# Kernel optimization log

Hardware: AMD Instinct MI355X
Metric: run time of the kernel (lower is better)

## Reference

```python
import jax, jax.numpy as jnp
import numpy as np


def setup_inputs() -> dict:
    key = jax.random.key(0)
    N, E, H, V, C, D, L = 10000, 50000, 128, 8, 5, 59, 2
    keys = iter(jax.random.split(key, 64))

    def p(*shape):
        return jax.random.normal(next(keys), shape, jnp.float32) * 0.05

    inp = dict(
        edge_index=jax.random.randint(next(keys), (2, E), 0, N),
        edge_attr=jax.random.normal(next(keys), (E, D), jnp.float32),
        delta_t=jnp.array([60.0], jnp.float32),
        memory=jnp.ones((N, H), jnp.float32),
        # edge_embed
        W_ee=p(H, D), b_ee=p(H),
        # edge_weight_gen
        W_ewg=p(V, 2 * H), b_ewg=p(V),
        # multi-view GIN convs (L layers, shared MLP across views)
        gin_W1=p(L, H, H), gin_b1=p(L, H), gin_W2=p(L, H, H), gin_b2=p(L, H),
        # Bochner time encoder
        W_t=p(H, 1), b_t=p(H),
        # GRUCell (torch gate order r,z,n)
        W_ih=p(3 * H, H), b_ih=p(3 * H), W_hh=p(3 * H, H), b_hh=p(3 * H),
        # update_nn (feeds detached memory only; not in returned outputs)
        W_up=p(H, V * H), b_up=p(H),
        # local attention (kdim=vdim=2H, 1 head)
        Wq_l=p(H, H), bq_l=p(H), Wk_l=p(H, 2 * H), bk_l=p(H),
        Wv_l=p(H, 2 * H), bv_l=p(H), Wo_l=p(H, H), bo_l=p(H),
        # global attention (1 head)
        Wq_g=p(H, H), bq_g=p(H), Wk_g=p(H, H), bk_g=p(H),
        Wv_g=p(H, H), bv_g=p(H), Wo_g=p(H, H), bo_g=p(H),
        # classifier MLP
        Wc1=p(H, 3 * H), bc1=p(H), Wc2=p(C, H), bc2=p(C),
    )
    return inp


def reference(edge_index, edge_attr, delta_t, memory,
              W_ee, b_ee, W_ewg, b_ewg,
              gin_W1, gin_b1, gin_W2, gin_b2,
              W_t, b_t, W_ih, b_ih, W_hh, b_hh, W_up, b_up,
              Wq_l, bq_l, Wk_l, bk_l, Wv_l, bv_l, Wo_l, bo_l,
              Wq_g, bq_g, Wk_g, bk_g, Wv_g, bv_g, Wo_g, bo_g,
              Wc1, bc1, Wc2, bc2):
    relu = jax.nn.relu
    N, H = memory.shape
    V = W_ewg.shape[0]
    L = gin_W1.shape[0]

    # ---- snapshot encoder (MultiGraphLayer) ----
    ea = relu(edge_attr @ W_ee.T + b_ee)                               # [E,H]
    src0, dst0 = edge_index[0], edge_index[1]
    ew = jax.nn.sigmoid(
        jnp.concatenate([ea, memory[src0]], -1) @ W_ewg.T + b_ewg)     # [E,V]
    h = jnp.broadcast_to(memory[:, None, :], (N, V, H))                # [N,V,H]
    cs, cd = dst0, src0  # edge_index flipped before convs (edge_index[[1,0]])
    for l in range(L):
        # multi-view GIN: view-weighted message + residual MLP update
        msg = relu(h[cs] + ea[:, None, :]) * ew[:, :, None]            # [E,V,H]
        agg = jax.ops.segment_sum(msg, cd, num_segments=N)             # [N,V,H]
        upd = relu((h + agg) @ gin_W1[l].T + gin_b1[l]) @ gin_W2[l].T + gin_b2[l]
        h = h + upd
    h_before = h

    # ---- GRU memory update (vectorized over the V 'class' slots) ----
    te = jnp.sin(delta_t[:, None] * W_t[:, 0] + b_t)                   # [1,H]
    x_in = h + te                                                      # [N,V,H]
    gi = x_in @ W_ih.T + b_ih                                          # [N,V,3H]
    gh = (memory @ W_hh.T + b_hh)[:, None, :]                          # [N,1,3H]
    r = jax.nn.sigmoid(gi[..., :H] + gh[..., :H])
    z = jax.nn.sigmoid(gi[..., H:2 * H] + gh[..., H:2 * H])
    n = jnp.tanh(gi[..., 2 * H:] + r * gh[..., 2 * H:])
    h_new = (1.0 - z) * n + z * memory[:, None, :]                     # [N,V,H]

    # ---- global/local attention fusion ----
    scale = 1.0 / jnp.sqrt(jnp.asarray(H, jnp.float32))
    sf, df = h_new[src0], h_new[dst0]                                  # [E,V,H]
    Wk1, Wk2 = Wk_l[:, :H], Wk_l[:, H:]  # split cat([src,dst]) projection
    Wv1, Wv2 = Wv_l[:, :H], Wv_l[:, H:]
    q_l = ea @ Wq_l.T + bq_l                                           # [E,H]
    K_l = sf @ Wk1.T + df @ Wk2.T + bk_l                               # [E,V,H]
    V_l = sf @ Wv1.T + df @ Wv2.T + bv_l
    a_l = jax.nn.softmax(jnp.einsum('eh,evh->ev', q_l, K_l) * scale, -1)
    local_out = jnp.einsum('ev,evh->eh', a_l, V_l) @ Wo_l.T + bo_l     # [E,H]

    pooled = h_new.mean(axis=0)                                        # [V,H]
    q_g = ea @ Wq_g.T + bq_g
    K_g = pooled @ Wk_g.T + bk_g
    V_g = pooled @ Wv_g.T + bv_g
    a_g = jax.nn.softmax((q_g @ K_g.T) * scale, axis=-1)               # [E,V]
    global_out = (a_g @ V_g) @ Wo_g.T + bo_g                           # [E,H]

    combined = jnp.concatenate([ea, local_out, global_out], axis=-1)   # [E,3H]
    logits = relu(combined @ Wc1.T + bc1) @ Wc2.T + bc2                # [E,C]
    return (logits, ew, h_before, a_g[:, None, :])
```

## Files before the change

kernel.cpp:

```cpp
#include <hip/hip_runtime.h>
#include <cstddef>


#define HSZ 128
typedef unsigned short ushortT;
typedef unsigned int uintT;
typedef short short8 __attribute__((ext_vector_type(8)));
typedef float f32x4 __attribute__((ext_vector_type(4)));

__device__ __forceinline__ float sigm(float x) { return 1.f / (1.f + __expf(-x)); }

__device__ __forceinline__ ushortT f2bf(float f) {
  unsigned int u = __float_as_uint(f);
  u += 0x7fffu + ((u >> 16) & 1u);
  return (ushortT)(u >> 16);
}
__device__ __forceinline__ float bf2f(ushortT u) {
  return __uint_as_float(((unsigned int)u) << 16);
}
__device__ __forceinline__ float bflo(uintT u) { return __uint_as_float(u << 16); }
__device__ __forceinline__ float bfhi(uintT u) { return __uint_as_float(u & 0xffff0000u); }
__device__ __forceinline__ uintT pk2bf(float a, float b) {
  return ((uintT)f2bf(b) << 16) | (uintT)f2bf(a);
}

__device__ __forceinline__ int swzA(int row, int chunk) {
  return row * 64 + (((chunk ^ row) & 7) << 3);
}
__device__ __forceinline__ int swzT(int row, int chunk) {
  return row * 128 + (((chunk & 8) | ((chunk ^ row) & 7)) << 3);
}

template<int ASRC, int ACT, bool OUTBF, bool ABF, bool WBF>
__global__ __launch_bounds__(256) void gemm_bf(
    const void* __restrict__ A1, const void* __restrict__ A2, const void* __restrict__ A3,
    const void* __restrict__ W, const float* __restrict__ bias,
    void* __restrict__ out_, int M, int K, int Nout)
{
  __shared__ short Ash[128 * 64];
  __shared__ short Bsh[128 * 64];
  float* out = (float*)out_;
  ushortT* outh = (ushortT*)out_;
  const int tid = threadIdx.x;
  const int m0 = blockIdx.x * 128;
  const int n0 = blockIdx.y * 128;
  const int l = tid & 63, w = tid >> 6;
  const int wr = w >> 1, wc = w & 1;
  const int lr = l & 15, lq = l >> 4;
  f32x4 acc[4][4] = {};

  for (int k0 = 0; k0 < K; k0 += 64) {
    __syncthreads();
    const bool fast = (k0 + 64 <= K);
    #pragma unroll
    for (int i = 0; i < 4; ++i) {
      int c = i * 256 + tid;
      int row = c >> 3, seg = c & 7;
      int kb = k0 + seg * 8;
      {
        int m = m0 + row;
        short8 pk;
        if (ABF) {
          if (m < M) {
            if (ASRC == 4) {
              if (kb < 128)
                pk = *reinterpret_cast<const short8*>((const ushortT*)A1 + (size_t)m * 128 + kb);
              else if (kb < 384)
                pk = *reinterpret_cast<const short8*>((const ushortT*)A2 + (size_t)m * 256 + (kb - 128));
              else
                pk = *reinterpret_cast<const short8*>((const ushortT*)A3 + (size_t)m * 128 + (kb - 384));
            } else {
              pk = *reinterpret_cast<const short8*>((const ushortT*)A1 + (size_t)m * K + kb);
            }
          } else {
            #pragma unroll
            for (int j = 0; j < 8; ++j) pk[j] = 0;
          }
        } else {
          const float* A1f = (const float*)A1;
          float v[8];
          if (fast && m < M) {
            const float4* p = reinterpret_cast<const float4*>(A1f + (size_t)m * K + kb);
            float4 x0 = p[0], x1 = p[1];
            v[0]=x0.x; v[1]=x0.y; v[2]=x0.z; v[3]=x0.w;
            v[4]=x1.x; v[5]=x1.y; v[6]=x1.z; v[7]=x1.w;
          } else {
            #pragma unroll
            for (int j = 0; j < 8; ++j) {
              int k = kb + j;
              v[j] = (m < M && k < K) ? A1f[(size_t)m * K + k] : 0.f;
            }
          }
          #pragma unroll
          for (int j = 0; j < 8; ++j) pk[j] = (short)f2bf(v[j]);
        }
        *reinterpret_cast<short8*>(&Ash[swzA(row, seg)]) = pk;
      }
      {
        int nn = n0 + row;
        short8 pk;
        if (WBF) {
          if (nn < Nout)
            pk = *reinterpret_cast<const short8*>((const ushortT*)W + (size_t)nn * K + kb);
          else {
            #pragma unroll
            for (int j = 0; j < 8; ++j) pk[j] = 0;
          }
        } else {
          const float* Wf = (const float*)W;
          float v[8];
          if (fast && nn < Nout) {
            const float4* p = reinterpret_cast<const float4*>(Wf + (size_t)nn * K + kb);
            float4 x0 = p[0], x1 = p[1];
            v[0]=x0.x; v[1]=x0.y; v[2]=x0.z; v[3]=x0.w;
            v[4]=x1.x; v[5]=x1.y; v[6]=x1.z; v[7]=x1.w;
          } else {
            #pragma unroll
            for (int j = 0; j < 8; ++j) {
              int k = kb + j;
              v[j] = (nn < Nout && k < K) ? Wf[(size_t)nn * K + k] : 0.f;
            }
          }
          #pragma unroll
          for (int j = 0; j < 8; ++j) pk[j] = (short)f2bf(v[j]);
        }
        *reinterpret_cast<short8*>(&Bsh[swzA(row, seg)]) = pk;
      }
    }
    __syncthreads();
    #pragma unroll
    for (int ks = 0; ks < 2; ++ks) {
      short8 a[4], b[4];
      #pragma unroll
      for (int mi = 0; mi < 4; ++mi)
        a[mi] = *reinterpret_cast<const short8*>(&Ash[swzA(wr*64 + mi*16 + lr, ks*4 + lq)]);
      #pragma unroll
      for (int ni = 0; ni < 4; ++ni)
        b[ni] = *reinterpret_cast<const short8*>(&Bsh[swzA(wc*64 + ni*16 + lr, ks*4 + lq)]);
      #pragma unroll
      for (int mi = 0; mi < 4; ++mi)
        #pragma unroll
        for (int ni = 0; ni < 4; ++ni)
          acc[mi][ni] = __builtin_amdgcn_mfma_f32_16x16x32_bf16(a[mi], b[ni], acc[mi][ni], 0, 0, 0);
    }
  }
  #pragma unroll
  for (int ni = 0; ni < 4; ++ni) {
    int col = n0 + wc*64 + ni*16 + lr;
    if (col >= Nout) continue;
    float bz = bias ? bias[col] : 0.f;
    #pragma unroll
    for (int mi = 0; mi < 4; ++mi) {
      int mb = m0 + wr*64 + mi*16 + lq*4;
      #pragma unroll
      for (int r = 0; r < 4; ++r) {
        int m = mb + r;
        if (m >= M) continue;
        float vv = acc[mi][ni][r] + bz;
        if (ACT == 1) vv = fmaxf(vv, 0.f);
        size_t o = (size_t)m * Nout + col;
        if (OUTBF) outh[o] = f2bf(vv); else out[o] = vv;
      }
    }
  }
}

template<int LMODE>
__global__ __launch_bounds__(256) void k_gin(
    const ushortT* __restrict__ hb, const ushortT* __restrict__ aggb,
    float* __restrict__ houtf, ushortT* __restrict__ houtb,
    const ushortT* __restrict__ W1b, const float* __restrict__ b1,
    const ushortT* __restrict__ W2b, const float* __restrict__ b2, int M)
{
  __shared__ short Tsh[16384];
  const int tid = threadIdx.x;
  const int m0 = blockIdx.x * 128;
  const int l = tid & 63, w = tid >> 6;
  const int wr = w >> 1, wc = w & 1;
  const int lr = l & 15, lq = l >> 4;
  f32x4 acc[4][4] = {};

  #pragma unroll
  for (int kk = 0; kk < 4; ++kk) {
    const int kof = kk * 32 + lq * 8;
    short8 a[4], b[4];
    #pragma unroll
    for (int mi = 0; mi < 4; ++mi) {
      int m = m0 + wr*64 + mi*16 + lr;
      if (m < M) {
        short8 hv;
        if (LMODE == 1) hv = *reinterpret_cast<const short8*>(hb + ((size_t)(m >> 3)) * 128 + kof);
        else            hv = *reinterpret_cast<const short8*>(hb + (size_t)m * 128 + kof);
        short8 av = *reinterpret_cast<const short8*>(aggb + (size_t)m * 128 + kof);
        #pragma unroll
        for (int j = 0; j < 8; ++j)
          a[mi][j] = (short)f2bf(bf2f((ushortT)hv[j]) + bf2f((ushortT)av[j]));
      } else {
        #pragma unroll
        for (int j = 0; j < 8; ++j) a[mi][j] = 0;
      }
    }
    #pragma unroll
    for (int ni = 0; ni < 4; ++ni)
      b[ni] = *reinterpret_cast<const short8*>(W1b + (size_t)(wc*64 + ni*16 + lr) * 128 + kof);
    #pragma unroll
    for (int mi = 0; mi < 4; ++mi)
      #pragma unroll
      for (int ni = 0; ni < 4; ++ni)
        acc[mi][ni] = __builtin_amdgcn_mfma_f32_16x16x32_bf16(a[mi], b[ni], acc[mi][ni], 0, 0, 0);
  }
  {
    float b1v[4];
    #pragma unroll
    for (int ni = 0; ni < 4; ++ni) b1v[ni] = b1[wc*64 + ni*16 + lr];
    #pragma unroll
    for (int mi = 0; mi < 4; ++mi)
      #pragma unroll
      for (int ni = 0; ni < 4; ++ni) {
        int col = wc*64 + ni*16 + lr;
        #pragma unroll
        for (int r = 0; r < 4; ++r) {
          int row = wr*64 + mi*16 + lq*4 + r;
          float v = fmaxf(acc[mi][ni][r] + b1v[ni], 0.f);
          Tsh[swzT(row, col >> 3) + (col & 7)] = (short)f2bf(v);
        }
      }
  }
  __syncthreads();
  f32x4 acc2[4][4] = {};
  #pragma unroll
  for (int kk = 0; kk < 4; ++kk) {
    const int kof = kk * 32 + lq * 8;
    short8 a[4], b[4];
    #pragma unroll
    for (int mi = 0; mi < 4; ++mi)
      a[mi] = *reinterpret_cast<const short8*>(&Tsh[swzT(wr*64 + mi*16 + lr, kk*4 + lq)]);
    #pragma unroll
    for (int ni = 0; ni < 4; ++ni)
      b[ni] = *reinterpret_cast<const short8*>(W2b + (size_t)(wc*64 + ni*16 + lr) * 128 + kof);
    #pragma unroll
    for (int mi = 0; mi < 4; ++mi)
      #pragma unroll
      for (int ni = 0; ni < 4; ++ni)
        acc2[mi][ni] = __builtin_amdgcn_mfma_f32_16x16x32_bf16(a[mi], b[ni], acc2[mi][ni], 0, 0, 0);
  }
  {
    float b2v[4];
    #pragma unroll
    for (int ni = 0; ni < 4; ++ni) b2v[ni] = b2[wc*64 + ni*16 + lr];
    #pragma unroll
    for (int ni = 0; ni < 4; ++ni) {
      int col = wc*64 + ni*16 + lr;
      #pragma unroll
      for (int mi = 0; mi < 4; ++mi) {
        int mb = m0 + wr*64 + mi*16 + lq*4;
        #pragma unroll
        for (int r = 0; r < 4; ++r) {
          int m = mb + r;
          if (m >= M) continue;
          float base = (LMODE == 1) ? bf2f(hb[((size_t)(m >> 3)) * 128 + col])
                                    : bf2f(hb[(size_t)m * 128 + col]);
          float ho = base + acc2[mi][ni][r] + b2v[ni];
          if (LMODE == 1) houtb[(size_t)m * 128 + col] = f2bf(ho);
          else            houtf[(size_t)m * 128 + col] = ho;
        }
      }
    }
  }
}

__global__ __launch_bounds__(512) void k_giru(
    const float* __restrict__ hf, const float* __restrict__ te,
    const ushortT* __restrict__ Wihb, const float* __restrict__ b_ih,
    const ushortT* __restrict__ ghb, const ushortT* __restrict__ memb,
    ushortT* __restrict__ hnb, float* __restrict__ prw, int M)
{
  __shared__ short Ash[8192];
  __shared__ float poolsh[1024];
  const int tid = threadIdx.x;
  const int m0 = blockIdx.x * 64;
  const int l = tid & 63, w = tid >> 6;
  const int lr = l & 15, lq = l >> 4;
  const int r0 = (w >> 1) * 16, c0 = (w & 1) * 64;
  f32x4 acc[3][4] = {};

  #pragma unroll
  for (int i = 0; i < 2; ++i) {
    int c = i * 512 + tid;
    int row = c >> 4, seg = c & 15;
    int m = m0 + row;
    short8 pk;
    if (m < M) {
      const float4* p = reinterpret_cast<const float4*>(hf + (size_t)m * 128 + seg * 8);
      const float4* t = reinterpret_cast<const float4*>(te + seg * 8);
      float4 x0 = p[0], x1 = p[1], t0 = t[0], t1 = t[1];
      pk[0]=(short)f2bf(x0.x+t0.x); pk[1]=(short)f2bf(x0.y+t0.y);
      pk[2]=(short)f2bf(x0.z+t0.z); pk[3]=(short)f2bf(x0.w+t0.w);
      pk[4]=(short)f2bf(x1.x+t1.x); pk[5]=(short)f2bf(x1.y+t1.y);
      pk[6]=(short)f2bf(x1.z+t1.z); pk[7]=(short)f2bf(x1.w+t1.w);
    } else {
      #pragma unroll
      for (int j = 0; j < 8; ++j) pk[j] = 0;
    }
    *reinterpret_cast<short8*>(&Ash[swzT(row, seg)]) = pk;
  }
  for (int i = tid; i < 1024; i += 512) poolsh[i] = 0.f;
  __syncthreads();
  #pragma unroll
  for (int kk = 0; kk < 4; ++kk) {
    short8 a = *reinterpret_cast<const short8*>(&Ash[swzT(r0 + lr, kk*4 + lq)]);
    #pragma unroll
    for (int s = 0; s < 3; ++s)
      #pragma unroll
      for (int xi = 0; xi < 4; ++xi) {
        short8 b = *reinterpret_cast<const short8*>(
            Wihb + (size_t)(s*128 + c0 + xi*16 + lr) * 128 + kk*32 + lq*8);
        acc[s][xi] = __builtin_amdgcn_mfma_f32_16x16x32_bf16(a, b, acc[s][xi], 0, 0, 0);
      }
  }
  #pragma unroll
  for (int xi = 0; xi < 4; ++xi) {
    int x = c0 + xi * 16 + lr;
    float br = b_ih[x], bz = b_ih[128 + x], bn = b_ih[256 + x];
    #pragma unroll
    for (int rr = 0; rr < 4; ++rr) {
      int m = m0 + r0 + lq * 4 + rr;
      if (m >= M) continue;
      int node = m >> 3;
      float ghr = bf2f(ghb[(size_t)node * 384 + x]);
      float ghz = bf2f(ghb[(size_t)node * 384 + 128 + x]);
      float ghn = bf2f(ghb[(size_t)node * 384 + 256 + x]);
      float mem = bf2f(memb[(size_t)node * 128 + x]);
      float rv = sigm(acc[0][xi][rr] + br + ghr);
      float zv = sigm(acc[1][xi][rr] + bz + ghz);
      float nv = tanhf(acc[2][xi][rr] + bn + rv * ghn);
      float hn = (1.f - zv) * nv + zv * mem;
      hnb[(size_t)m * 128 + x] = f2bf(hn);
      atomicAdd(&poolsh[(m & 7) * 128 + x], hn);
    }
  }
  __syncthreads();
  for (int i = tid; i < 1024; i += 512) atomicAdd(&prw[i], poolsh[i]);
}

__global__ void k_hist(const int* __restrict__ srcI, int* __restrict__ cnt, int E)
{
  int e = blockIdx.x * 256 + threadIdx.x;
  if (e < E) atomicAdd(&cnt[srcI[e]], 1);
}

__global__ __launch_bounds__(1024) void k_scan(const int* __restrict__ cnt,
    int* __restrict__ ofs, int* __restrict__ cur, int N)
{
  __shared__ int buf[1024];
  __shared__ int carry;
  int tid = threadIdx.x;
  if (tid == 0) carry = 0;
  __syncthreads();
  for (int base = 0; base < N; base += 1024) {
    int i = base + tid;
    int v = (i < N) ? cnt[i] : 0;
    buf[tid] = v;
    __syncthreads();
    for (int off = 1; off < 1024; off <<= 1) {
      int t = (tid >= off) ? buf[tid - off] : 0;
      __syncthreads();
      buf[tid] += t;
      __syncthreads();
    }
    int excl = carry + buf[tid] - v;
    if (i < N) { ofs[i] = excl; cur[i] = excl; }
    __syncthreads();
    if (tid == 0) carry += buf[1023];
    __syncthreads();
  }
  if (tid == 0) ofs[N] = carry;
}

__global__ void k_fill(const int* __restrict__ srcI, int* __restrict__ cur,
                       int* __restrict__ eid, int E)
{
  int e = blockIdx.x * 256 + threadIdx.x;
  if (e >= E) return;
  int p = atomicAdd(&cur[srcI[e]], 1);
  eid[p] = e;
}

template<int LMODE>
__global__ __launch_bounds__(256) void k_agg(const ushortT* __restrict__ hb,
    const ushortT* __restrict__ eab, const float* __restrict__ ew,
    const int* __restrict__ dstI, const int* __restrict__ ofs,
    const int* __restrict__ eid, ushortT* __restrict__ aggb, int N)
{
  int half = threadIdx.x >> 7;
  int x = threadIdx.x & 127;
  int n = blockIdx.x * 2 + half;
  if (n >= N) return;
  float acc[8] = {};
  int beg = ofs[n], end = ofs[n + 1];
  for (int i = beg; i < end; ++i) {
    int e = eid[i];
    int d = dstI[e];
    float eav = bf2f(eab[(size_t)e * 128 + x]);
    const float* ewp = ew + (size_t)e * 8;
    if (LMODE == 1) {
      float m = fmaxf(bf2f(hb[(size_t)d * 128 + x]) + eav, 0.f);
      #pragma unroll
      for (int v = 0; v < 8; ++v) acc[v] += m * ewp[v];
    } else {
      const ushortT* hd = hb + (size_t)d * 1024;
      #pragma unroll
      for (int v = 0; v < 8; ++v)
        acc[v] += fmaxf(bf2f(hd[v * 128 + x]) + eav, 0.f) * ewp[v];
    }
  }
  ushortT* ag = aggb + (size_t)n * 1024;
  #pragma unroll
  for (int v = 0; v < 8; ++v) ag[v * 128 + x] = f2bf(acc[v]);
}

__global__ __launch_bounds__(256) void k_ew(const ushortT* __restrict__ eab,
    const ushortT* __restrict__ memb, const int* __restrict__ srcI,
    const float* __restrict__ W_ewg, const float* __restrict__ b_ewg,
    float* __restrict__ ew, int E)
{
  __shared__ float Wsh[2048];
  __shared__ float bsh[8];
  int tid = threadIdx.x;
  for (int i = tid; i < 2048; i += 256) Wsh[i] = W_ewg[i];
  if (tid < 8) bsh[tid] = b_ewg[tid];
  __syncthreads();
  int wv = tid >> 6, lane = tid & 63;
  int e = blockIdx.x * 4 + wv;
  if (e >= E) return;
  int s = srcI[e];
  float c0 = bf2f(eab[(size_t)e * 128 + lane]);
  float c1 = bf2f(eab[(size_t)e * 128 + 64 + lane]);
  float c2 = bf2f(memb[(size_t)s * 128 + lane]);
  float c3 = bf2f(memb[(size_t)s * 128 + 64 + lane]);
  #pragma unroll
  for (int v = 0; v < 8; ++v) {
    float p = c0 * Wsh[v * 256 + lane] + c1 * Wsh[v * 256 + 64 + lane]
            + c2 * Wsh[v * 256 + 128 + lane] + c3 * Wsh[v * 256 + 192 + lane];
    #pragma unroll
    for (int o = 32; o; o >>= 1) p += __shfl_down(p, o);
    if (lane == 0) ew[(size_t)e * 8 + v] = sigm(p + bsh[v]);
  }
}

__global__ void k_cvtall(const float* __restrict__ s0, ushortT* __restrict__ d0, int n0,
                         const float* __restrict__ s1, ushortT* __restrict__ d1, int n1,
                         const float* __restrict__ s2, ushortT* __restrict__ d2, int n2,
                         const float* __restrict__ s3, ushortT* __restrict__ d3, int n3)
{
  int i = blockIdx.x * 256 + threadIdx.x;
  if (i < n0) { d0[i] = f2bf(s0[i]); return; }
  i -= n0;
  if (i < n1) { d1[i] = f2bf(s1[i]); return; }
  i -= n1;
  if (i < n2) { d2[i] = f2bf(s2[i]); return; }
  i -= n2;
  if (i < n3) d3[i] = f2bf(s3[i]);
}

__global__ __launch_bounds__(256) void k_prep(
    const float* __restrict__ Wo_l, const float* __restrict__ Wv_l,
    const float* __restrict__ bv_l, const float* __restrict__ bo_l,
    const float* __restrict__ Wq_l, const float* __restrict__ bq_l,
    const float* __restrict__ Wk_l,
    const float* __restrict__ delta_t, const float* __restrict__ W_t,
    const float* __restrict__ b_t,
    float* __restrict__ Wl2f, float* __restrict__ blv,
    ushortT* __restrict__ Wqkgb, float* __restrict__ bqkg, float* __restrict__ te)
{
  int idx = blockIdx.x * 256 + threadIdx.x;
  if (idx < 32768) {
    int n = idx >> 8, k = idx & 255;
    float a = 0.f;
    for (int j = 0; j < 128; ++j) a += Wo_l[n * 128 + j] * Wv_l[j * 256 + k];
    Wl2f[idx] = a;
  } else {
    int rem = idx - 32768;
    int n = rem >> 7, j = rem & 127;
    float a = 0.f;
    for (int k = 0; k < 128; ++k) a += Wq_l[k * 128 + j] * Wk_l[k * 256 + n];
    Wqkgb[rem] = f2bf(a);
  }
  if (blockIdx.x == 0 && threadIdx.x < 128) {
    int n = threadIdx.x;
    float a = bo_l[n];
    for (int j = 0; j < 128; ++j) a += Wo_l[n * 128 + j] * bv_l[j];
    blv[n] = a;
  }
  if (blockIdx.x == 1) {
    int n = threadIdx.x;
    float a = 0.f;
    for (int k = 0; k < 128; ++k) a += bq_l[k] * Wk_l[k * 256 + n];
    bqkg[n] = a;
  }
  if (blockIdx.x == 2 && threadIdx.x < 128) {
    int t = threadIdx.x;
    te[t] = sinf(delta_t[0] * W_t[t] + b_t[t]);
  }
}

__global__ __launch_bounds__(256) void k_prep2(
    const float* __restrict__ Wc1, const float* __restrict__ bc1,
    const float* __restrict__ Wl2f, const float* __restrict__ blv,
    ushortT* __restrict__ Wc1p, float* __restrict__ bc1p)
{
  int idx = blockIdx.x * 256 + threadIdx.x;
  int n = idx >> 9, k = idx & 511;
  float a;
  if (k < 128) a = Wc1[(size_t)n * 384 + k];
  else if (k < 384) {
    int kk = k - 128;
    a = 0.f;
    for (int j = 0; j < 128; ++j) a += Wc1[(size_t)n * 384 + 128 + j] * Wl2f[j * 256 + kk];
  } else a = Wc1[(size_t)n * 384 + 256 + (k - 384)];
  Wc1p[idx] = f2bf(a);
  if (blockIdx.x == 0 && threadIdx.x < 128) {
    int nn = threadIdx.x;
    float b = bc1[nn];
    for (int j = 0; j < 128; ++j) b += Wc1[(size_t)nn * 384 + 128 + j] * blv[j];
    bc1p[nn] = b;
  }
}

__global__ __launch_bounds__(256) void k_kgg(const float* __restrict__ prw,
    const float* __restrict__ Wk_g, const float* __restrict__ Wv_g, const float* __restrict__ bv_g,
    const float* __restrict__ Wo_g, float* __restrict__ Kg, float* __restrict__ G, int N)
{
  __shared__ float pl[1024];
  __shared__ float vg[1024];
  int tid = threadIdx.x;
  float invN = 1.f / (float)N;
  for (int i = tid; i < 1024; i += 256) pl[i] = prw[i] * invN;
  __syncthreads();
  for (int o = tid; o < 1024; o += 256) {
    int v = o >> 7, x = o & 127;
    float a = 0.f, b = 0.f;
    for (int k = 0; k < 128; ++k) {
      float p = pl[v * 128 + k];
      a += p * Wk_g[(size_t)x * 128 + k];
      b += p * Wv_g[(size_t)x * 128 + k];
    }
    Kg[o] = a;
    vg[o] = b + bv_g[x];
  }
  __syncthreads();
  for (int o = tid; o < 1024; o += 256) {
    int v = o >> 7, x = o & 127;
    float a = 0.f;
    for (int k = 0; k < 128; ++k) a += vg[v * 128 + k] * Wo_g[(size_t)x * 128 + k];
    G[o] = a;
  }
}

__global__ __launch_bounds__(256) void k_sc(const float* __restrict__ Kg,
    const float* __restrict__ Wq_g, const float* __restrict__ bq_g,
    ushortT* __restrict__ Wqkgb, float* __restrict__ bqkg)
{
  int idx = blockIdx.x * 256 + threadIdx.x;
  int v = idx >> 7, j = idx & 127;
  float a = 0.f;
  for (int x = 0; x < 128; ++x) a += Kg[v * 128 + x] * Wq_g[(size_t)x * 128 + j];
  Wqkgb[(size_t)(256 + v) * 128 + j] = f2bf(a);
  if (blockIdx.x == 0 && threadIdx.x < 8) {
    int vv = threadIdx.x;
    float b = 0.f;
    for (int x = 0; x < 128; ++x) b += bq_g[x] * Kg[vv * 128 + x];
    bqkg[256 + vv] = b;
  }
}

__global__ __launch_bounds__(256) void k_lg(
    const ushortT* __restrict__ hnb, const ushortT* __restrict__ qkgb,
    const int* __restrict__ srcI, const int* __restrict__ dstI,
    const float* __restrict__ G, const float* __restrict__ bo_g,
    float* __restrict__ ag_out, ushortT* __restrict__ wsd,
    ushortT* __restrict__ glbb, int E)
{
  __shared__ float Gs[1024], bsh[128];
  int tid = threadIdx.x;
  for (int i = tid; i < 1024; i += 256) Gs[i] = G[i];
  if (tid < 128) bsh[tid] = bo_g[tid];
  __syncthreads();
  int w = tid >> 6, l = tid & 63, half = l >> 5, l31 = l & 31;
  int e = blockIdx.x * 8 + w * 2 + half;
  int ec = (e < E) ? e : (E - 1);
  int s = srcI[ec], d = dstI[ec];
  const uint2* qrow = reinterpret_cast<const uint2*>(qkgb + (size_t)ec * 264);
  uint2 q1u = qrow[l31], q2u = qrow[32 + l31];
  uint4 scu = *reinterpret_cast<const uint4*>(qkgb + (size_t)ec * 264 + 256);
  const uint2* srow = reinterpret_cast<const uint2*>(hnb + (size_t)s * 1024);
  const uint2* drow = reinterpret_cast<const uint2*>(hnb + (size_t)d * 1024);
  uint2 su[8], du[8];
  #pragma unroll
  for (int v = 0; v < 8; ++v) { su[v] = srow[v * 32 + l31]; du[v] = drow[v * 32 + l31]; }
  float q1f[4] = {bflo(q1u.x), bfhi(q1u.x), bflo(q1u.y), bfhi(q1u.y)};
  float q2f[4] = {bflo(q2u.x), bfhi(q2u.x), bflo(q2u.y), bfhi(q2u.y)};
  float pl[8];
  #pragma unroll
  for (int v = 0; v < 8; ++v) {
    pl[v] = q1f[0] * bflo(su[v].x) + q1f[1] * bfhi(su[v].x)
          + q1f[2] * bflo(su[v].y) + q1f[3] * bfhi(su[v].y)
          + q2f[0] * bflo(du[v].x) + q2f[1] * bfhi(du[v].x)
          + q2f[2] * bflo(du[v].y) + q2f[3] * bfhi(du[v].y);
  }
  #pragma unroll
  for (int v = 0; v < 8; ++v) {
    #pragma unroll
    for (int m = 1; m <= 16; m <<= 1) pl[v] += __shfl_xor(pl[v], m);
  }
  const float scale = 0.08838834764831845f;
  float mx = fmaxf(fmaxf(fmaxf(pl[0], pl[1]), fmaxf(pl[2], pl[3])),
                   fmaxf(fmaxf(pl[4], pl[5]), fmaxf(pl[6], pl[7])));
  float suml = 0.f, al[8];
  #pragma unroll
  for (int v = 0; v < 8; ++v) { al[v] = __expf((pl[v] - mx) * scale); suml += al[v]; }
  float invl = 1.f / suml;
  float ws0 = 0.f, ws1 = 0.f, ws2 = 0.f, ws3 = 0.f;
  float wd0 = 0.f, wd1 = 0.f, wd2 = 0.f, wd3 = 0.f;
  #pragma unroll
  for (int v = 0; v < 8; ++v) {
    float a = al[v];
    ws0 += a * bflo(su[v].x); ws1 += a * bfhi(su[v].x);
    ws2 += a * bflo(su[v].y); ws3 += a * bfhi(su[v].y);
    wd0 += a * bflo(du[v].x); wd1 += a * bfhi(du[v].x);
    wd2 += a * bflo(du[v].y); wd3 += a * bfhi(du[v].y);
  }
  if (e < E) {
    uint2* wrow = reinterpret_cast<uint2*>(wsd + (size_t)e * 256);
    uint2 t0; t0.x = pk2bf(ws0 * invl, ws1 * invl); t0.y = pk2bf(ws2 * invl, ws3 * invl);
    uint2 t1; t1.x = pk2bf(wd0 * invl, wd1 * invl); t1.y = pk2bf(wd2 * invl, wd3 * invl);
    wrow[l31] = t0;
    wrow[32 + l31] = t1;
  }
  float sg[8] = {bflo(scu.x), bfhi(scu.x), bflo(scu.y), bfhi(scu.y),
                 bflo(scu.z), bfhi(scu.z), bflo(scu.w), bfhi(scu.w)};
  float mg = fmaxf(fmaxf(fmaxf(sg[0], sg[1]), fmaxf(sg[2], sg[3])),
                   fmaxf(fmaxf(sg[4], sg[5]), fmaxf(sg[6], sg[7])));
  float sumg = 0.f, ag[8];
  #pragma unroll
  for (int v = 0; v < 8; ++v) { ag[v] = __expf((sg[v] - mg) * scale); sumg += ag[v]; }
  float invg = 1.f / sumg;
  if (e < E && l31 < 8) ag_out[(size_t)e * 8 + l31] = ag[l31] * invg;
  float4 b4 = *reinterpret_cast<const float4*>(&bsh[4 * l31]);
  float g0 = b4.x, g1 = b4.y, g2 = b4.z, g3 = b4.w;
  #pragma unroll
  for (int v = 0; v < 8; ++v) {
    float sv = ag[v] * invg;
    float4 gv = *reinterpret_cast<const float4*>(&Gs[v * 128 + 4 * l31]);
    g0 += sv * gv.x; g1 += sv * gv.y; g2 += sv * gv.z; g3 += sv * gv.w;
  }
  if (e < E) {
    uint2 t; t.x = pk2bf(g0, g1); t.y = pk2bf(g2, g3);
    reinterpret_cast<uint2*>(glbb + (size_t)e * 128)[l31] = t;
  }
}

__global__ __launch_bounds__(256) void k_logits(const ushortT* __restrict__ hid,
    const float* __restrict__ Wc2, const float* __restrict__ bc2,
    float* __restrict__ logits, int E)
{
  __shared__ float Wsh[640];
  __shared__ float bsh[5];
  int tid = threadIdx.x;
  for (int i = tid; i < 640; i += 256) Wsh[i] = Wc2[i];
  if (tid < 5) bsh[tid] = bc2[tid];
  __syncthreads();
  int wv = tid >> 6, lane = tid & 63;
  int e = blockIdx.x * 4 + wv;
  if (e >= E) return;
  float h0 = bf2f(hid[(size_t)e * 128 + lane]), h1 = bf2f(hid[(size_t)e * 128 + 64 + lane]);
  #pragma unroll
  for (int c = 0; c < 5; ++c) {
    float p = h0 * Wsh[c * 128 + lane] + h1 * Wsh[c * 128 + 64 + lane];
    #pragma unroll
    for (int o = 32; o; o >>= 1) p += __shfl_down(p, o);
    if (lane == 0) logits[(size_t)e * 5 + c] = p + bsh[c];
  }
}

extern "C" void kernel_launch(void* const* d_in, const int* in_sizes, int n_in,
                              void* d_out, int out_size, void* d_ws, size_t ws_size,
                              hipStream_t stream)
{
  const int*   edge_index = (const int*)d_in[0];
  const float* edge_attr  = (const float*)d_in[1];
  const float* delta_t    = (const float*)d_in[2];
  const float* memory     = (const float*)d_in[3];
  const float* W_ee  = (const float*)d_in[4];
  const float* b_ee  = (const float*)d_in[5];
  const float* W_ewg = (const float*)d_in[6];
  const float* b_ewg = (const float*)d_in[7];
  const float* gin_W1 = (const float*)d_in[8];
  const float* gin_b1 = (const float*)d_in[9];
  const float* gin_W2 = (const float*)d_in[10];
  const float* gin_b2 = (const float*)d_in[11];
  const float* W_t  = (const float*)d_in[12];
  const float* b_t  = (const float*)d_in[13];
  const float* W_ih = (const float*)d_in[14];
  const float* b_ih = (const float*)d_in[15];
  const float* W_hh = (const float*)d_in[16];
  const float* b_hh = (const float*)d_in[17];
  const float* Wq_l = (const float*)d_in[20];
  const float* bq_l = (const float*)d_in[21];
  const float* Wk_l = (const float*)d_in[22];
  const float* Wv_l = (const float*)d_in[24];
  const float* bv_l = (const float*)d_in[25];
  const float* Wo_l = (const float*)d_in[26];
  const float* bo_l = (const float*)d_in[27];
  const float* Wq_g = (const float*)d_in[28];
  const float* bq_g = (const float*)d_in[29];
  const float* Wk_g = (const float*)d_in[30];
  const float* Wv_g = (const float*)d_in[32];
  const float* bv_g = (const float*)d_in[33];
  const float* Wo_g = (const float*)d_in[34];
  const float* bo_g = (const float*)d_in[35];
  const float* Wc1  = (const float*)d_in[36];
  const float* bc1  = (const float*)d_in[37];
  const float* Wc2  = (const float*)d_in[38];
  const float* bc2  = (const float*)d_in[39];

  const int E = in_sizes[0] / 2;
  const int N = in_sizes[3] / HSZ;
  const int* srcI = edge_index;
  const int* dstI = edge_index + E;

  float* out    = (float*)d_out;
  float* logits = out;
  float* ew     = out + (size_t)E * 5;
  float* h      = out + (size_t)E * 13;
  float* ag_out = out + (size_t)E * 13 + (size_t)N * 1024;

  float* ws = (float*)d_ws;
  size_t off = 0;
  auto alloc = [&](size_t n) { size_t o = off; off += (n + 255) & ~(size_t)255; return o; };
  float* te   = ws + alloc(128);
  float* blv  = ws + alloc(128);
  float* bqkg = ws + alloc(384);
  float* bc1p = ws + alloc(128);
  float* Kg   = ws + alloc(1024);
  float* G    = ws + alloc(1024);
  float* prw  = ws + alloc(1024);
  int* cnt = (int*)(ws + alloc(N));
  int* ofs = (int*)(ws + alloc(N + 1));
  int* cur = (int*)(ws + alloc(N));
  int* eid = (int*)(ws + alloc(E));
  ushortT* memb   = (ushortT*)(ws + alloc((size_t)N * 64));
  ushortT* eab    = (ushortT*)(ws + alloc((size_t)E * 64));
  ushortT* h1b    = (ushortT*)(ws + alloc((size_t)N * 512));
  ushortT* hnb    = (ushortT*)(ws + alloc((size_t)N * 512));
  ushortT* ghb    = (ushortT*)(ws + alloc((size_t)N * 192));
  ushortT* ginW1b = (ushortT*)(ws + alloc(16384));
  ushortT* ginW2b = (ushortT*)(ws + alloc(16384));
  ushortT* Wihb   = (ushortT*)(ws + alloc(24576));
  float*   Wl2f   = ws + alloc(32768);
  ushortT* Wc1p   = (ushortT*)(ws + alloc(32768));
  ushortT* Wqkgb  = (ushortT*)(ws + alloc(16896));
  size_t brA = (size_t)N * 512, brC = (size_t)E * 324;
  size_t brsz = brA > brC ? brA : brC;
  float* BR = ws + alloc(brsz);
  if (ws_size < off * sizeof(float)) return;

  ushortT* aggb = (ushortT*)BR;
  ushortT* qkgb = (ushortT*)BR;
  ushortT* wsd  = (ushortT*)(BR + (size_t)E * 132);
  ushortT* glbb = (ushortT*)(BR + (size_t)E * 260);
  ushortT* hid  = (ushortT*)BR;

  auto cdiv = [](int a, int b) { return (a + b - 1) / b; };

  hipMemsetAsync(cnt, 0, (size_t)N * sizeof(int), stream);
  hipMemsetAsync(prw, 0, 1024 * sizeof(float), stream);
  k_hist<<<cdiv(E, 256), 256, 0, stream>>>(srcI, cnt, E);
  k_scan<<<1, 1024, 0, stream>>>(cnt, ofs, cur, N);
  k_fill<<<cdiv(E, 256), 256, 0, stream>>>(srcI, cur, eid, E);
  {
    int total = N * 128 + 32768 + 32768 + 49152;
    k_cvtall<<<cdiv(total, 256), 256, 0, stream>>>(
        memory, memb, N * 128, gin_W1, ginW1b, 32768,
        gin_W2, ginW2b, 32768, W_ih, Wihb, 49152);
  }
  gemm_bf<0, 1, true, false, false><<<dim3(cdiv(E, 128), 1), 256, 0, stream>>>(
      edge_attr, nullptr, nullptr, W_ee, b_ee, eab, E, 59, 128);
  k_ew<<<cdiv(E, 4), 256, 0, stream>>>(eab, memb, srcI, W_ewg, b_ewg, ew, E);
  k_prep<<<256, 256, 0, stream>>>(Wo_l, Wv_l, bv_l, bo_l, Wq_l, bq_l, Wk_l,
                                  delta_t, W_t, b_t, Wl2f, blv, Wqkgb, bqkg, te);
  k_prep2<<<256, 256, 0, stream>>>(Wc1, bc1, Wl2f, blv, Wc1p, bc1p);
  gemm_bf<0, 0, true, false, false><<<dim3(cdiv(N, 128), 3), 256, 0, stream>>>(
      memory, nullptr, nullptr, W_hh, b_hh, ghb, N, 128, 384);
  k_agg<1><<<cdiv(N, 2), 256, 0, stream>>>(memb, eab, ew, dstI, ofs, eid, aggb, N);
  k_gin<1><<<cdiv(N * 8, 128), 256, 0, stream>>>(
      memb, aggb, nullptr, h1b, ginW1b, gin_b1, ginW2b, gin_b2, N * 8);
  k_agg<2><<<cdiv(N, 2), 256, 0, stream>>>(h1b, eab, ew, dstI, ofs, eid, aggb, N);
  k_gin<2><<<cdiv(N * 8, 128), 256, 0, stream>>>(
      h1b, aggb, h, nullptr, ginW1b + 16384, gin_b1 + 128,
      ginW2b + 16384, gin_b2 + 128, N * 8);
  k_giru<<<cdiv(N * 8, 64), 512, 0, stream>>>(h, te, Wihb, b_ih, ghb, memb, hnb, prw, N * 8);
  k_kgg<<<1, 256, 0, stream>>>(prw, Wk_g, Wv_g, bv_g, Wo_g, Kg, G, N);
  k_sc<<<4, 256, 0, stream>>>(Kg, Wq_g, bq_g, Wqkgb, bqkg);
  gemm_bf<0, 0, true, true, true><<<dim3(cdiv(E, 128), 3), 256, 0, stream>>>(
      eab, nullptr, nullptr, Wqkgb, bqkg, qkgb, E, 128, 264);
  k_lg<<<cdiv(E, 8), 256, 0, stream>>>(hnb, qkgb, srcI, dstI, G, bo_g,
                                       ag_out, wsd, glbb, E);
  gemm_bf<4, 1, true, true, true><<<dim3(cdiv(E, 128), 1), 256, 0, stream>>>(
      eab, wsd, glbb, Wc1p, bc1p, hid, E, 512, 128);
  k_logits<<<cdiv(E, 4), 256, 0, stream>>>(hid, Wc2, bc2, logits, E);
}
```

Baseline: 562.3 us.

## Stage GRU input weights in LDS and move mean pooling to separate kernel

```diff
diff --git a/kernel.cpp b/kernel.cpp
--- a/kernel.cpp
+++ b/kernel.cpp
@@ -273,10 +273,9 @@
     const float* __restrict__ hf, const float* __restrict__ te,
     const ushortT* __restrict__ Wihb, const float* __restrict__ b_ih,
     const ushortT* __restrict__ ghb, const ushortT* __restrict__ memb,
-    ushortT* __restrict__ hnb, float* __restrict__ prw, int M)
-{
-  __shared__ short Ash[8192];
-  __shared__ float poolsh[1024];
+    ushortT* __restrict__ hnb, int M)
+{
+  __shared__ short Bsh[24576];
   const int tid = threadIdx.x;
   const int m0 = blockIdx.x * 64;
   const int l = tid & 63, w = tid >> 6;
@@ -284,39 +283,42 @@
   const int r0 = (w >> 1) * 16, c0 = (w & 1) * 64;
   f32x4 acc[3][4] = {};
 
-  #pragma unroll
-  for (int i = 0; i < 2; ++i) {
-    int c = i * 512 + tid;
-    int row = c >> 4, seg = c & 15;
-    int m = m0 + row;
-    short8 pk;
-    if (m < M) {
-      const float4* p = reinterpret_cast<const float4*>(hf + (size_t)m * 128 + seg * 8);
-      const float4* t = reinterpret_cast<const float4*>(te + seg * 8);
-      float4 x0 = p[0], x1 = p[1], t0 = t[0], t1 = t[1];
-      pk[0]=(short)f2bf(x0.x+t0.x); pk[1]=(short)f2bf(x0.y+t0.y);
-      pk[2]=(short)f2bf(x0.z+t0.z); pk[3]=(short)f2bf(x0.w+t0.w);
-      pk[4]=(short)f2bf(x1.x+t1.x); pk[5]=(short)f2bf(x1.y+t1.y);
-      pk[6]=(short)f2bf(x1.z+t1.z); pk[7]=(short)f2bf(x1.w+t1.w);
-    } else {
-      #pragma unroll
-      for (int j = 0; j < 8; ++j) pk[j] = 0;
-    }
-    *reinterpret_cast<short8*>(&Ash[swzT(row, seg)]) = pk;
-  }
-  for (int i = tid; i < 1024; i += 512) poolsh[i] = 0.f;
-  __syncthreads();
-  #pragma unroll
-  for (int kk = 0; kk < 4; ++kk) {
-    short8 a = *reinterpret_cast<const short8*>(&Ash[swzT(r0 + lr, kk*4 + lq)]);
-    #pragma unroll
-    for (int s = 0; s < 3; ++s)
-      #pragma unroll
-      for (int xi = 0; xi < 4; ++xi) {
-        short8 b = *reinterpret_cast<const short8*>(
-            Wihb + (size_t)(s*128 + c0 + xi*16 + lr) * 128 + kk*32 + lq*8);
-        acc[s][xi] = __builtin_amdgcn_mfma_f32_16x16x32_bf16(a, b, acc[s][xi], 0, 0, 0);
+  for (int ks2 = 0; ks2 < 2; ++ks2) {
+    if (ks2) __syncthreads();
+    #pragma unroll
+    for (int i = 0; i < 6; ++i) {
+      int c = i * 512 + tid;
+      int row = c >> 3, seg = c & 7;
+      *reinterpret_cast<short8*>(&Bsh[swzA(row, seg)]) =
+          *reinterpret_cast<const short8*>(Wihb + (size_t)row * 128 + ks2 * 64 + seg * 8);
+    }
+    __syncthreads();
+    #pragma unroll
+    for (int ks = 0; ks < 2; ++ks) {
+      int m = m0 + r0 + lr;
+      int kof = ks2 * 64 + ks * 32 + lq * 8;
+      short8 a;
+      if (m < M) {
+        const float4* p = reinterpret_cast<const float4*>(hf + (size_t)m * 128 + kof);
+        const float4* t = reinterpret_cast<const float4*>(te + kof);
+        float4 x0 = p[0], x1 = p[1], t0 = t[0], t1 = t[1];
+        a[0]=(short)f2bf(x0.x+t0.x); a[1]=(short)f2bf(x0.y+t0.y);
+        a[2]=(short)f2bf(x0.z+t0.z); a[3]=(short)f2bf(x0.w+t0.w);
+        a[4]=(short)f2bf(x1.x+t1.x); a[5]=(short)f2bf(x1.y+t1.y);
+        a[6]=(short)f2bf(x1.z+t1.z); a[7]=(short)f2bf(x1.w+t1.w);
+      } else {
+        #pragma unroll
+        for (int j = 0; j < 8; ++j) a[j] = 0;
       }
+      #pragma unroll
+      for (int s = 0; s < 3; ++s)
+        #pragma unroll
+        for (int xi = 0; xi < 4; ++xi) {
+          short8 b = *reinterpret_cast<const short8*>(
+              &Bsh[swzA(s*128 + c0 + xi*16 + lr, ks*4 + lq)]);
+          acc[s][xi] = __builtin_amdgcn_mfma_f32_16x16x32_bf16(a, b, acc[s][xi], 0, 0, 0);
+        }
+    }
   }
   #pragma unroll
   for (int xi = 0; xi < 4; ++xi) {
@@ -334,13 +336,23 @@
       float rv = sigm(acc[0][xi][rr] + br + ghr);
       float zv = sigm(acc[1][xi][rr] + bz + ghz);
       float nv = tanhf(acc[2][xi][rr] + bn + rv * ghn);
-      float hn = (1.f - zv) * nv + zv * mem;
-      hnb[(size_t)m * 128 + x] = f2bf(hn);
-      atomicAdd(&poolsh[(m & 7) * 128 + x], hn);
-    }
-  }
-  __syncthreads();
-  for (int i = tid; i < 1024; i += 512) atomicAdd(&prw[i], poolsh[i]);
+      hnb[(size_t)m * 128 + x] = f2bf((1.f - zv) * nv + zv * mem);
+    }
+  }
+}
+
+__global__ __launch_bounds__(256) void k_pool(const ushortT* __restrict__ hnb,
+                                              float* __restrict__ prw, int N)
+{
+  int tid = threadIdx.x;
+  float acc[4] = {0.f, 0.f, 0.f, 0.f};
+  for (int n = blockIdx.x; n < N; n += gridDim.x) {
+    const ushortT* row = hnb + (size_t)n * 1024;
+    #pragma unroll
+    for (int j = 0; j < 4; ++j) acc[j] += bf2f(row[tid + j * 256]);
+  }
+  #pragma unroll
+  for (int j = 0; j < 4; ++j) atomicAdd(&prw[tid + j * 256], acc[j]);
 }
 
 __global__ void k_hist(const int* __restrict__ srcI, int* __restrict__ cnt, int E)
@@ -799,7 +811,8 @@
   k_gin<2><<<cdiv(N * 8, 128), 256, 0, stream>>>(
       h1b, aggb, h, nullptr, ginW1b + 16384, gin_b1 + 128,
       ginW2b + 16384, gin_b2 + 128, N * 8);
-  k_giru<<<cdiv(N * 8, 64), 512, 0, stream>>>(h, te, Wihb, b_ih, ghb, memb, hnb, prw, N * 8);
+  k_giru<<<cdiv(N * 8, 64), 512, 0, stream>>>(h, te, Wihb, b_ih, ghb, memb, hnb, N * 8);
+  k_pool<<<256, 256, 0, stream>>>(hnb, prw, N);
   k_kgg<<<1, 256, 0, stream>>>(prw, Wk_g, Wv_g, bv_g, Wo_g, Kg, G, N);
   k_sc<<<4, 256, 0, stream>>>(Kg, Wq_g, bq_g, Wqkgb, bqkg);
   gemm_bf<0, 0, true, true, true><<<dim3(cdiv(E, 128), 3), 256, 0, stream>>>(
```

Measured after the change: 510.7 us (median of 3 runs). -9.2%, faster.
